# Performance work log

Measured on AMD Instinct MI355X. Metric: run time of the kernel, lower is better.

Reference implementation:

```python
import jax, jax.numpy as jnp
import numpy as np
import math

H = 768
NH = 12
D = H // NH


def setup_inputs() -> dict:
    key = jax.random.key(0)
    ks = jax.random.split(key, 13)
    B, S = 1, 384
    s = 0.02
    inp = {
        "hidden_states": jax.random.normal(ks[0], (B, S, H), jnp.float32),
        "attention_mask": jnp.zeros((B, 1, 1, S), jnp.float32),
        "pos_emb": jax.random.normal(ks[1], (B, S, S, H), jnp.float32),
        "Wq": jax.random.normal(ks[2], (H, H), jnp.float32) * s,
        "bq": jnp.zeros((H,), jnp.float32),
        "Wk": jax.random.normal(ks[3], (H, H), jnp.float32) * s,
        "bk": jnp.zeros((H,), jnp.float32),
        "Wv": jax.random.normal(ks[4], (H, H), jnp.float32) * s,
        "bv": jnp.zeros((H,), jnp.float32),
        "Wpk": jax.random.normal(ks[5], (H, H), jnp.float32) * s,
        "bpk": jnp.zeros((H,), jnp.float32),
        "Wpq": jax.random.normal(ks[6], (H, H), jnp.float32) * s,
        "bpq": jnp.zeros((H,), jnp.float32),
    }
    return inp


def reference(hidden_states, attention_mask, pos_emb,
              Wq, bq, Wk, bk, Wv, bv, Wpk, bpk, Wpq, bpq):
    B, S, Hd = hidden_states.shape
    split = lambda x: x.reshape(B, S, NH, D).transpose(0, 2, 1, 3)  # -> (B, h, S, d)
    q = split(hidden_states @ Wq + bq)
    k = split(hidden_states @ Wk + bk)
    v = split(hidden_states @ Wv + bv)

    # content-to-content
    c2c = jnp.einsum('bhid,bhjd->bhij', q, k)

    # per-pair position projections: (B,S,S,H) -> (B,S,S,h,d)
    pos_key = (pos_emb @ Wpk + bpk).reshape(B, S, S, NH, D)
    pos_query = (pos_emb @ Wpq + bpq).reshape(B, S, S, NH, D)

    # content-to-position: q[b,h,i,:] . pos_key[b,i,j,h,:]
    c2p = jnp.einsum('bhid,bijhd->bhij', q, pos_key)
    # position-to-content: pos_query[b,j,i,h,:] . k[b,h,j,:]
    p2c = jnp.einsum('bjihd,bhjd->bhij', pos_query, k)

    scores = (c2c + c2p + p2c) / math.sqrt(D) + attention_mask
    probs = jax.nn.softmax(scores, axis=-1)  # dropout is identity (p=0 / eval)
    ctx = jnp.einsum('bhij,bhjd->bhid', probs, v)
    return ctx.transpose(0, 2, 1, 3).reshape(B, S, Hd)
```

## Files before the change

kernel.cpp:

```cpp
#include <hip/hip_runtime.h>
#include <math.h>

#define SEQ 384
#define HDIM 768
#define NHEAD 12
#define DHEAD 64

__global__ __launch_bounds__(256)
void qkv_gemm(const float* __restrict__ X,
              const float* __restrict__ Wq, const float* __restrict__ bq,
              const float* __restrict__ Wk, const float* __restrict__ bk,
              const float* __restrict__ Wv, const float* __restrict__ bv,
              float* __restrict__ q, float* __restrict__ k, float* __restrict__ v)
{
    __shared__ float Xs[16][68];
    __shared__ float Ws[16][68];
    const int z = blockIdx.z;
    const float* W    = (z == 0) ? Wq : (z == 1) ? Wk : Wv;
    const float* bias = (z == 0) ? bq : (z == 1) ? bk : bv;
    float* out        = (z == 0) ? q  : (z == 1) ? k  : v;

    const int m0 = blockIdx.x * 64;
    const int n0 = blockIdx.y * 64;
    const int tid = threadIdx.x;
    const int ty = tid / 16, tx = tid % 16;

    const int lxm = tid / 4,  lxk = (tid % 4) * 4;
    const int lwk = tid / 16, lwn = (tid % 16) * 4;

    float acc[4][4] = {};

    for (int k0 = 0; k0 < HDIM; k0 += 16) {
        float4 xa = *(const float4*)&X[(m0 + lxm) * HDIM + k0 + lxk];
        float4 wa = *(const float4*)&W[(size_t)(k0 + lwk) * HDIM + n0 + lwn];
        __syncthreads();
        Xs[lxk + 0][lxm] = xa.x; Xs[lxk + 1][lxm] = xa.y;
        Xs[lxk + 2][lxm] = xa.z; Xs[lxk + 3][lxm] = xa.w;
        *(float4*)&Ws[lwk][lwn] = wa;
        __syncthreads();
        #pragma unroll
        for (int kk = 0; kk < 16; kk++) {
            float4 a4 = *(const float4*)&Xs[kk][4 * ty];
            float4 b4 = *(const float4*)&Ws[kk][4 * tx];
            float a[4] = {a4.x, a4.y, a4.z, a4.w};
            float b[4] = {b4.x, b4.y, b4.z, b4.w};
            #pragma unroll
            for (int ia = 0; ia < 4; ia++)
                #pragma unroll
                for (int ib = 0; ib < 4; ib++)
                    acc[ia][ib] = fmaf(a[ia], b[ib], acc[ia][ib]);
        }
    }
    float4 bv4 = *(const float4*)&bias[n0 + 4 * tx];
    #pragma unroll
    for (int ia = 0; ia < 4; ia++) {
        float4 o;
        o.x = acc[ia][0] + bv4.x; o.y = acc[ia][1] + bv4.y;
        o.z = acc[ia][2] + bv4.z; o.w = acc[ia][3] + bv4.w;
        *(float4*)&out[(size_t)(m0 + 4 * ty + ia) * HDIM + n0 + 4 * tx] = o;
    }
}

__global__ __launch_bounds__(256)
void pos_proj(const float* __restrict__ q, const float* __restrict__ k,
              const float* __restrict__ Wpk, const float* __restrict__ Wpq,
              float* __restrict__ qp, float* __restrict__ kp)
{
    __shared__ float As[64][68];
    __shared__ float Bs[64][68];
    const int h = blockIdx.z % NHEAD;
    const int s = blockIdx.z / NHEAD;
    const float* Asrc = s ? k   : q;
    const float* Wsrc = s ? Wpq : Wpk;
    float* out        = s ? kp  : qp;

    const int i0 = blockIdx.x * 64, e0 = blockIdx.y * 64;
    const int tid = threadIdx.x;
    const int dg = tid % 16, row = tid / 16;

    #pragma unroll
    for (int r = 0; r < 4; r++) {
        const int rr = r * 16 + row;
        float4 a4 = *(const float4*)&Asrc[(size_t)(i0 + rr) * HDIM + h * 64 + dg * 4];
        float4 b4 = *(const float4*)&Wsrc[(size_t)(e0 + rr) * HDIM + h * 64 + dg * 4];
        As[dg * 4 + 0][rr] = a4.x; As[dg * 4 + 1][rr] = a4.y;
        As[dg * 4 + 2][rr] = a4.z; As[dg * 4 + 3][rr] = a4.w;
        Bs[dg * 4 + 0][rr] = b4.x; Bs[dg * 4 + 1][rr] = b4.y;
        Bs[dg * 4 + 2][rr] = b4.z; Bs[dg * 4 + 3][rr] = b4.w;
    }
    __syncthreads();

    const int ty = tid / 16, tx = tid % 16;
    float acc[4][4] = {};
    #pragma unroll 4
    for (int d = 0; d < 64; d++) {
        float4 a4 = *(const float4*)&As[d][4 * ty];
        float4 b4 = *(const float4*)&Bs[d][4 * tx];
        float a[4] = {a4.x, a4.y, a4.z, a4.w};
        float b[4] = {b4.x, b4.y, b4.z, b4.w};
        #pragma unroll
        for (int ia = 0; ia < 4; ia++)
            #pragma unroll
            for (int ib = 0; ib < 4; ib++)
                acc[ia][ib] = fmaf(a[ia], b[ib], acc[ia][ib]);
    }
    #pragma unroll
    for (int ia = 0; ia < 4; ia++) {
        float4 o = make_float4(acc[ia][0], acc[ia][1], acc[ia][2], acc[ia][3]);
        *(float4*)&out[((size_t)(i0 + 4 * ty + ia) * NHEAD + h) * HDIM + e0 + 4 * tx] = o;
    }
}

__global__ __launch_bounds__(256)
void scores_pos(const float* __restrict__ pe, const float* __restrict__ qp,
                const float* __restrict__ kp,
                float* __restrict__ A1, float* __restrict__ P2T)
{
    __shared__ float lds[32 * 388];
    const int i    = blockIdx.x;
    const int tid  = threadIdx.x;
    const int lane = tid & 63;
    const int wave = tid >> 6;
    const int rgu = __builtin_amdgcn_readfirstlane(wave >> 1);
    const int esu = __builtin_amdgcn_readfirstlane(wave & 1);

    const float* pebase = pe + (size_t)i * SEQ * HDIM;
    const float* wb = (rgu ? kp : qp) + (size_t)i * NHEAD * HDIM;

    const int wr  = tid >> 3;
    const int wec = tid & 7;

    float acc[12][6] = {};

    for (int c = 0; c < 24; c++) {
        const int e0 = c * 32;
        __syncthreads();
        #pragma unroll
        for (int rnd = 0; rnd < 6; rnd++) {
            const int jb = rnd * 64 + wr * 2;
            float4 g0 = *(const float4*)&pebase[(size_t)jb * HDIM + e0 + wec * 4];
            float4 g1 = *(const float4*)&pebase[(size_t)(jb + 1) * HDIM + e0 + wec * 4];
            *(float2*)&lds[(wec * 4 + 0) * 388 + jb] = make_float2(g0.x, g1.x);
            *(float2*)&lds[(wec * 4 + 1) * 388 + jb] = make_float2(g0.y, g1.y);
            *(float2*)&lds[(wec * 4 + 2) * 388 + jb] = make_float2(g0.z, g1.z);
            *(float2*)&lds[(wec * 4 + 3) * 388 + jb] = make_float2(g0.w, g1.w);
        }
        __syncthreads();
        const float* wc = wb + e0 + esu * 16;
        #pragma unroll 4
        for (int ee = 0; ee < 16; ee++) {
            const int ei = esu * 16 + ee;
            float4 p4 = *(const float4*)&lds[ei * 388 + lane * 4];
            float2 p2 = *(const float2*)&lds[ei * 388 + 256 + lane * 2];
            #pragma unroll
            for (int r = 0; r < 12; r++) {
                const float w = wc[r * HDIM + ee];
                acc[r][0] = fmaf(w, p4.x, acc[r][0]);
                acc[r][1] = fmaf(w, p4.y, acc[r][1]);
                acc[r][2] = fmaf(w, p4.z, acc[r][2]);
                acc[r][3] = fmaf(w, p4.w, acc[r][3]);
                acc[r][4] = fmaf(w, p2.x, acc[r][4]);
                acc[r][5] = fmaf(w, p2.y, acc[r][5]);
            }
        }
    }

    __syncthreads();
    if (esu == 1) {
        #pragma unroll
        for (int r = 0; r < 12; r++) {
            const int row = rgu * 12 + r;
            *(float4*)&lds[row * 392 + lane * 4] =
                make_float4(acc[r][0], acc[r][1], acc[r][2], acc[r][3]);
            *(float2*)&lds[row * 392 + 256 + lane * 2] =
                make_float2(acc[r][4], acc[r][5]);
        }
    }
    __syncthreads();
    if (esu == 0) {
        #pragma unroll
        for (int r = 0; r < 12; r++) {
            const int row = rgu * 12 + r;
            float4 o4 = *(const float4*)&lds[row * 392 + lane * 4];
            float2 o2 = *(const float2*)&lds[row * 392 + 256 + lane * 2];
            o4.x += acc[r][0]; o4.y += acc[r][1]; o4.z += acc[r][2]; o4.w += acc[r][3];
            o2.x += acc[r][4]; o2.y += acc[r][5];
            *(float4*)&lds[row * 392 + lane * 4] = o4;
            *(float2*)&lds[row * 392 + 256 + lane * 2] = o2;
        }
    }
    __syncthreads();

    for (int t = tid; t < 24 * 96; t += 256) {
        const int row = t / 96;
        const int c4  = (t % 96) * 4;
        float4 o = *(const float4*)&lds[row * 392 + c4];
        float* dst = (row < 12)
            ? &A1[((size_t)row * SEQ + i) * SEQ + c4]
            : &P2T[((size_t)(row - 12) * SEQ + i) * SEQ + c4];
        *(float4*)dst = o;
    }
}

__global__ __launch_bounds__(384)
void attn_out(const float* __restrict__ A1, const float* __restrict__ P2T,
              const float* __restrict__ q, const float* __restrict__ k,
              const float* __restrict__ v,
              const float* __restrict__ bpk, const float* __restrict__ bpq,
              const float* __restrict__ mask, float* __restrict__ out)
{
    const int i = blockIdx.x, h = blockIdx.y;
    const int tid = threadIdx.x;
    __shared__ float q_s[64], bk_s[64], bq_s[64];
    __shared__ float p_s[SEQ];
    __shared__ float redm[6], reds[6], redv[6 * 64];

    if (tid < 64)       q_s[tid]        = q[(size_t)i * HDIM + h * 64 + tid];
    else if (tid < 128) bk_s[tid - 64]  = bpk[h * 64 + tid - 64];
    else if (tid < 192) bq_s[tid - 128] = bpq[h * 64 + tid - 128];
    __syncthreads();

    const float* kr = k + (size_t)tid * HDIM + h * 64;
    float c2c = 0.f, kb = 0.f;
    #pragma unroll
    for (int dd = 0; dd < 16; dd++) {
        float4 k4 = *(const float4*)(kr + 4 * dd);
        c2c = fmaf(q_s[4 * dd + 0], k4.x, c2c);
        c2c = fmaf(q_s[4 * dd + 1], k4.y, c2c);
        c2c = fmaf(q_s[4 * dd + 2], k4.z, c2c);
        c2c = fmaf(q_s[4 * dd + 3], k4.w, c2c);
        kb  = fmaf(bq_s[4 * dd + 0], k4.x, kb);
        kb  = fmaf(bq_s[4 * dd + 1], k4.y, kb);
        kb  = fmaf(bq_s[4 * dd + 2], k4.z, kb);
        kb  = fmaf(bq_s[4 * dd + 3], k4.w, kb);
    }
    float qb = 0.f;
    #pragma unroll 8
    for (int d = 0; d < 64; d++) qb = fmaf(q_s[d], bk_s[d], qb);

    float sc = (A1[((size_t)h * SEQ + i) * SEQ + tid] +
                P2T[((size_t)h * SEQ + tid) * SEQ + i] +
                c2c + kb + qb) * 0.125f + mask[tid];

    const int lane = tid & 63, w = tid >> 6;
    float m = sc;
    #pragma unroll
    for (int o = 32; o; o >>= 1) m = fmaxf(m, __shfl_xor(m, o));
    if (lane == 0) redm[w] = m;
    __syncthreads();
    m = redm[0];
    #pragma unroll
    for (int t = 1; t < 6; t++) m = fmaxf(m, redm[t]);

    float p = __expf(sc - m);
    float sum = p;
    #pragma unroll
    for (int o = 32; o; o >>= 1) sum += __shfl_xor(sum, o);
    if (lane == 0) reds[w] = sum;
    p_s[tid] = p;
    __syncthreads();
    const float SUM = reds[0] + reds[1] + reds[2] + reds[3] + reds[4] + reds[5];

    float accv = 0.f;
    const float* vbase = v + h * 64 + lane;
    const int j0 = w * 64;
    #pragma unroll 8
    for (int jj = 0; jj < 64; jj++)
        accv = fmaf(p_s[j0 + jj], vbase[(size_t)(j0 + jj) * HDIM], accv);
    redv[w * 64 + lane] = accv;
    __syncthreads();
    if (tid < 64) {
        float o = redv[tid] + redv[64 + tid] + redv[128 + tid] +
                  redv[192 + tid] + redv[256 + tid] + redv[320 + tid];
        out[(size_t)i * HDIM + h * 64 + tid] = o / SUM;
    }
}

extern "C" void kernel_launch(void* const* d_in, const int* in_sizes, int n_in,
                              void* d_out, int out_size, void* d_ws, size_t ws_size,
                              hipStream_t stream)
{
    const float* hs   = (const float*)d_in[0];
    const float* mask = (const float*)d_in[1];
    const float* pe   = (const float*)d_in[2];
    const float* Wq   = (const float*)d_in[3];
    const float* bq   = (const float*)d_in[4];
    const float* Wk   = (const float*)d_in[5];
    const float* bk   = (const float*)d_in[6];
    const float* Wv   = (const float*)d_in[7];
    const float* bv   = (const float*)d_in[8];
    const float* Wpk  = (const float*)d_in[9];
    const float* bpk  = (const float*)d_in[10];
    const float* Wpq  = (const float*)d_in[11];
    const float* bpq  = (const float*)d_in[12];

    float* ws = (float*)d_ws;
    const size_t SZ_QKV = (size_t)SEQ * HDIM;
    const size_t SZ_QP  = (size_t)SEQ * NHEAD * HDIM;
    const size_t SZ_SC  = (size_t)NHEAD * SEQ * SEQ;
    float* q   = ws;
    float* k   = q  + SZ_QKV;
    float* v   = k  + SZ_QKV;
    float* qp  = v  + SZ_QKV;
    float* kp  = qp + SZ_QP;
    float* A1  = kp + SZ_QP;
    float* P2T = A1 + SZ_SC;

    qkv_gemm<<<dim3(6, 12, 3), 256, 0, stream>>>(hs, Wq, bq, Wk, bk, Wv, bv, q, k, v);
    pos_proj<<<dim3(6, 12, 24), 256, 0, stream>>>(q, k, Wpk, Wpq, qp, kp);
    scores_pos<<<dim3(SEQ), 256, 0, stream>>>(pe, qp, kp, A1, P2T);
    attn_out<<<dim3(SEQ, NHEAD), 384, 0, stream>>>(A1, P2T, q, k, v, bpk, bpq, mask,
                                                   (float*)d_out);
}
```

Baseline: 858.2 us.

## Split scores_pos over j halves, batch pe loads, restructure qkv and PV loops

scores_pos now launches a second grid dimension that splits the 384 j positions into two halves of 192. This doubles the block count and halves the per-block LDS footprint and register accumulators, and it issues all pe loads for a chunk before the barrier. qkv_gemm stages 128-wide K slabs of X in LDS and reads W directly from global memory with float4 loads. attn_out's PV product uses float4 loads of v across 16 lanes with a 24-way reduction. The aim is better occupancy and latency hiding on the dominant pos_emb streaming kernel. The cost is that each block re-reads the qp/kp weights.

```diff
diff --git a/kernel.cpp b/kernel.cpp
--- a/kernel.cpp
+++ b/kernel.cpp
@@ -13,8 +13,7 @@
               const float* __restrict__ Wv, const float* __restrict__ bv,
               float* __restrict__ q, float* __restrict__ k, float* __restrict__ v)
 {
-    __shared__ float Xs[16][68];
-    __shared__ float Ws[16][68];
+    __shared__ float Xs[128 * 68];
     const int z = blockIdx.z;
     const float* W    = (z == 0) ? Wq : (z == 1) ? Wk : Wv;
     const float* bias = (z == 0) ? bq : (z == 1) ? bk : bv;
@@ -25,23 +24,31 @@
     const int tid = threadIdx.x;
     const int ty = tid / 16, tx = tid % 16;
 
-    const int lxm = tid / 4,  lxk = (tid % 4) * 4;
-    const int lwk = tid / 16, lwn = (tid % 16) * 4;
+    const int lm = tid >> 2;
+    const int lc = (tid & 3) * 4;
 
     float acc[4][4] = {};
 
-    for (int k0 = 0; k0 < HDIM; k0 += 16) {
-        float4 xa = *(const float4*)&X[(m0 + lxm) * HDIM + k0 + lxk];
-        float4 wa = *(const float4*)&W[(size_t)(k0 + lwk) * HDIM + n0 + lwn];
+    for (int k0 = 0; k0 < HDIM; k0 += 128) {
+        float4 xa[8];
+        #pragma unroll
+        for (int it = 0; it < 8; it++)
+            xa[it] = *(const float4*)&X[(size_t)(m0 + lm) * HDIM + k0 + it * 16 + lc];
         __syncthreads();
-        Xs[lxk + 0][lxm] = xa.x; Xs[lxk + 1][lxm] = xa.y;
-        Xs[lxk + 2][lxm] = xa.z; Xs[lxk + 3][lxm] = xa.w;
-        *(float4*)&Ws[lwk][lwn] = wa;
+        #pragma unroll
+        for (int it = 0; it < 8; it++) {
+            const int kk = it * 16 + lc;
+            Xs[(kk + 0) * 68 + lm] = xa[it].x;
+            Xs[(kk + 1) * 68 + lm] = xa[it].y;
+            Xs[(kk + 2) * 68 + lm] = xa[it].z;
+            Xs[(kk + 3) * 68 + lm] = xa[it].w;
+        }
         __syncthreads();
-        #pragma unroll
-        for (int kk = 0; kk < 16; kk++) {
-            float4 a4 = *(const float4*)&Xs[kk][4 * ty];
-            float4 b4 = *(const float4*)&Ws[kk][4 * tx];
+        const float* Wp = &W[(size_t)k0 * HDIM + n0 + 4 * tx];
+        #pragma unroll 8
+        for (int kk = 0; kk < 128; kk++) {
+            float4 b4 = *(const float4*)&Wp[(size_t)kk * HDIM];
+            float4 a4 = *(const float4*)&Xs[kk * 68 + 4 * ty];
             float a[4] = {a4.x, a4.y, a4.z, a4.w};
             float b[4] = {b4.x, b4.y, b4.z, b4.w};
             #pragma unroll
@@ -116,51 +123,55 @@
                 const float* __restrict__ kp,
                 float* __restrict__ A1, float* __restrict__ P2T)
 {
-    __shared__ float lds[32 * 388];
+    __shared__ float lds[32 * 200];
     const int i    = blockIdx.x;
+    const int jh   = blockIdx.y;
     const int tid  = threadIdx.x;
     const int lane = tid & 63;
     const int wave = tid >> 6;
     const int rgu = __builtin_amdgcn_readfirstlane(wave >> 1);
     const int esu = __builtin_amdgcn_readfirstlane(wave & 1);
 
-    const float* pebase = pe + (size_t)i * SEQ * HDIM;
+    const float* pebase = pe + ((size_t)i * SEQ + jh * 192) * HDIM;
     const float* wb = (rgu ? kp : qp) + (size_t)i * NHEAD * HDIM;
 
     const int wr  = tid >> 3;
     const int wec = tid & 7;
 
-    float acc[12][6] = {};
+    float acc[12][3] = {};
 
     for (int c = 0; c < 24; c++) {
         const int e0 = c * 32;
+        float4 g[6];
+        #pragma unroll
+        for (int rnd = 0; rnd < 3; rnd++) {
+            const int jb = rnd * 64 + wr * 2;
+            g[2 * rnd + 0] = *(const float4*)&pebase[(size_t)jb * HDIM + e0 + wec * 4];
+            g[2 * rnd + 1] = *(const float4*)&pebase[(size_t)(jb + 1) * HDIM + e0 + wec * 4];
+        }
         __syncthreads();
         #pragma unroll
-        for (int rnd = 0; rnd < 6; rnd++) {
+        for (int rnd = 0; rnd < 3; rnd++) {
             const int jb = rnd * 64 + wr * 2;
-            float4 g0 = *(const float4*)&pebase[(size_t)jb * HDIM + e0 + wec * 4];
-            float4 g1 = *(const float4*)&pebase[(size_t)(jb + 1) * HDIM + e0 + wec * 4];
-            *(float2*)&lds[(wec * 4 + 0) * 388 + jb] = make_float2(g0.x, g1.x);
-            *(float2*)&lds[(wec * 4 + 1) * 388 + jb] = make_float2(g0.y, g1.y);
-            *(float2*)&lds[(wec * 4 + 2) * 388 + jb] = make_float2(g0.z, g1.z);
-            *(float2*)&lds[(wec * 4 + 3) * 388 + jb] = make_float2(g0.w, g1.w);
+            const float4 g0 = g[2 * rnd], g1 = g[2 * rnd + 1];
+            *(float2*)&lds[(wec * 4 + 0) * 200 + jb] = make_float2(g0.x, g1.x);
+            *(float2*)&lds[(wec * 4 + 1) * 200 + jb] = make_float2(g0.y, g1.y);
+            *(float2*)&lds[(wec * 4 + 2) * 200 + jb] = make_float2(g0.z, g1.z);
+            *(float2*)&lds[(wec * 4 + 3) * 200 + jb] = make_float2(g0.w, g1.w);
         }
         __syncthreads();
         const float* wc = wb + e0 + esu * 16;
         #pragma unroll 4
         for (int ee = 0; ee < 16; ee++) {
             const int ei = esu * 16 + ee;
-            float4 p4 = *(const float4*)&lds[ei * 388 + lane * 4];
-            float2 p2 = *(const float2*)&lds[ei * 388 + 256 + lane * 2];
+            float2 p2 = *(const float2*)&lds[ei * 200 + 2 * lane];
+            float  p1 = lds[ei * 200 + 128 + lane];
             #pragma unroll
             for (int r = 0; r < 12; r++) {
                 const float w = wc[r * HDIM + ee];
-                acc[r][0] = fmaf(w, p4.x, acc[r][0]);
-                acc[r][1] = fmaf(w, p4.y, acc[r][1]);
-                acc[r][2] = fmaf(w, p4.z, acc[r][2]);
-                acc[r][3] = fmaf(w, p4.w, acc[r][3]);
-                acc[r][4] = fmaf(w, p2.x, acc[r][4]);
-                acc[r][5] = fmaf(w, p2.y, acc[r][5]);
+                acc[r][0] = fmaf(w, p2.x, acc[r][0]);
+                acc[r][1] = fmaf(w, p2.y, acc[r][1]);
+                acc[r][2] = fmaf(w, p1,   acc[r][2]);
             }
         }
     }
@@ -170,10 +181,8 @@
         #pragma unroll
         for (int r = 0; r < 12; r++) {
             const int row = rgu * 12 + r;
-            *(float4*)&lds[row * 392 + lane * 4] =
-                make_float4(acc[r][0], acc[r][1], acc[r][2], acc[r][3]);
-            *(float2*)&lds[row * 392 + 256 + lane * 2] =
-                make_float2(acc[r][4], acc[r][5]);
+            *(float2*)&lds[row * 200 + 2 * lane] = make_float2(acc[r][0], acc[r][1]);
+            lds[row * 200 + 128 + lane] = acc[r][2];
         }
     }
     __syncthreads();
@@ -181,23 +190,22 @@
         #pragma unroll
         for (int r = 0; r < 12; r++) {
             const int row = rgu * 12 + r;
-            float4 o4 = *(const float4*)&lds[row * 392 + lane * 4];
-            float2 o2 = *(const float2*)&lds[row * 392 + 256 + lane * 2];
-            o4.x += acc[r][0]; o4.y += acc[r][1]; o4.z += acc[r][2]; o4.w += acc[r][3];
-            o2.x += acc[r][4]; o2.y += acc[r][5];
-            *(float4*)&lds[row * 392 + lane * 4] = o4;
-            *(float2*)&lds[row * 392 + 256 + lane * 2] = o2;
-        }
-    }
-    __syncthreads();
-
-    for (int t = tid; t < 24 * 96; t += 256) {
-        const int row = t / 96;
-        const int c4  = (t % 96) * 4;
-        float4 o = *(const float4*)&lds[row * 392 + c4];
+            float2 o2 = *(const float2*)&lds[row * 200 + 2 * lane];
+            float  o1 = lds[row * 200 + 128 + lane];
+            o2.x += acc[r][0]; o2.y += acc[r][1]; o1 += acc[r][2];
+            *(float2*)&lds[row * 200 + 2 * lane] = o2;
+            lds[row * 200 + 128 + lane] = o1;
+        }
+    }
+    __syncthreads();
+
+    for (int t = tid; t < 24 * 48; t += 256) {
+        const int row = t / 48;
+        const int c4  = (t % 48) * 4;
+        float4 o = *(const float4*)&lds[row * 200 + c4];
         float* dst = (row < 12)
-            ? &A1[((size_t)row * SEQ + i) * SEQ + c4]
-            : &P2T[((size_t)(row - 12) * SEQ + i) * SEQ + c4];
+            ? &A1[((size_t)row * SEQ + i) * SEQ + jh * 192 + c4]
+            : &P2T[((size_t)(row - 12) * SEQ + i) * SEQ + jh * 192 + c4];
         *(float4*)dst = o;
     }
 }
@@ -213,7 +221,8 @@
     const int tid = threadIdx.x;
     __shared__ float q_s[64], bk_s[64], bq_s[64];
     __shared__ float p_s[SEQ];
-    __shared__ float redm[6], reds[6], redv[6 * 64];
+    __shared__ float redm[6], reds[6];
+    __shared__ float redvf[24 * 64];
 
     if (tid < 64)       q_s[tid]        = q[(size_t)i * HDIM + h * 64 + tid];
     else if (tid < 128) bk_s[tid - 64]  = bpk[h * 64 + tid - 64];
@@ -261,17 +270,23 @@
     __syncthreads();
     const float SUM = reds[0] + reds[1] + reds[2] + reds[3] + reds[4] + reds[5];
 
-    float accv = 0.f;
-    const float* vbase = v + h * 64 + lane;
+    const int dq = lane & 15, jsub = lane >> 4;
     const int j0 = w * 64;
+    float4 av = make_float4(0.f, 0.f, 0.f, 0.f);
     #pragma unroll 8
-    for (int jj = 0; jj < 64; jj++)
-        accv = fmaf(p_s[j0 + jj], vbase[(size_t)(j0 + jj) * HDIM], accv);
-    redv[w * 64 + lane] = accv;
+    for (int jj = 0; jj < 16; jj++) {
+        const int j = j0 + jj * 4 + jsub;
+        float4 v4 = *(const float4*)&v[(size_t)j * HDIM + h * 64 + dq * 4];
+        const float pj = p_s[j];
+        av.x = fmaf(pj, v4.x, av.x); av.y = fmaf(pj, v4.y, av.y);
+        av.z = fmaf(pj, v4.z, av.z); av.w = fmaf(pj, v4.w, av.w);
+    }
+    *(float4*)&redvf[(w * 4 + jsub) * 64 + dq * 4] = av;
     __syncthreads();
     if (tid < 64) {
-        float o = redv[tid] + redv[64 + tid] + redv[128 + tid] +
-                  redv[192 + tid] + redv[256 + tid] + redv[320 + tid];
+        float o = 0.f;
+        #pragma unroll
+        for (int r = 0; r < 24; r++) o += redvf[r * 64 + tid];
         out[(size_t)i * HDIM + h * 64 + tid] = o / SUM;
     }
 }
@@ -308,7 +323,7 @@
 
     qkv_gemm<<<dim3(6, 12, 3), 256, 0, stream>>>(hs, Wq, bq, Wk, bk, Wv, bv, q, k, v);
     pos_proj<<<dim3(6, 12, 24), 256, 0, stream>>>(q, k, Wpk, Wpq, qp, kp);
-    scores_pos<<<dim3(SEQ), 256, 0, stream>>>(pe, qp, kp, A1, P2T);
+    scores_pos<<<dim3(SEQ, 2), 256, 0, stream>>>(pe, qp, kp, A1, P2T);
     attn_out<<<dim3(SEQ, NHEAD), 384, 0, stream>>>(A1, P2T, q, k, v, bpk, bpq, mask,
                                                    (float*)d_out);
 }
```

After: 845.1 us. Within noise of the previous version (-1.5%).
